# Kernel tuning notes

Measured on AMD Instinct MI355X. Metric: run time of the kernel, lower is better.

Reference implementation:

```python
import jax, jax.numpy as jnp
import numpy as np

N_NODES = 50000
N_EDGES = 800000
IN_FEATS = 256
H_FEATS = 256
NUM_CLASSES = 16
NUM_GRAPHS = 64


def _glorot(key, shape):
    lim = float(np.sqrt(6.0 / (shape[0] + shape[1])))
    return jax.random.uniform(key, shape, jnp.float32, -lim, lim)


def setup_inputs() -> dict:
    key = jax.random.key(0)
    ks = jax.random.split(key, 12)
    x = jax.random.normal(ks[0], (N_NODES, IN_FEATS), jnp.float32)
    edge_index = jax.random.randint(ks[1], (2, N_EDGES), 0, N_NODES, jnp.int64)
    batch_vec = jnp.sort(jax.random.randint(ks[2], (N_NODES,), 0, NUM_GRAPHS, jnp.int64))
    W1 = _glorot(ks[3], (IN_FEATS, H_FEATS)); b1 = jnp.zeros((H_FEATS,), jnp.float32)
    W2 = _glorot(ks[4], (H_FEATS, H_FEATS)); b2 = jnp.zeros((H_FEATS,), jnp.float32)
    W3 = _glorot(ks[5], (H_FEATS, H_FEATS)); b3 = jnp.zeros((H_FEATS,), jnp.float32)
    W4 = _glorot(ks[6], (H_FEATS, NUM_CLASSES)); b4 = jnp.zeros((NUM_CLASSES,), jnp.float32)
    return {"x": x, "edge_index": edge_index, "batch_vec": batch_vec,
            "W1": W1, "b1": b1, "W2": W2, "b2": b2,
            "W3": W3, "b3": b3, "W4": W4, "b4": b4}


def gcn_conv(x, W, b, src, dst, deg_inv_sqrt):
    # PyG GCNConv: out = D^{-1/2} (A + I) D^{-1/2} (x W) + b
    h = x @ W  # [N, F_out]
    norm = deg_inv_sqrt[src] * deg_inv_sqrt[dst]  # [E+N]
    msgs = h[src] * norm[:, None]  # gather + scale
    agg = jax.ops.segment_sum(msgs, dst, num_segments=x.shape[0])
    return agg + b


def reference(x, edge_index, batch_vec, W1, b1, W2, b2, W3, b3, W4, b4):
    n = x.shape[0]
    # add self-loops once (shared across layers)
    loops = jnp.arange(n, dtype=edge_index.dtype)
    src = jnp.concatenate([edge_index[0], loops])
    dst = jnp.concatenate([edge_index[1], loops])
    deg = jax.ops.segment_sum(jnp.ones_like(dst, dtype=x.dtype), dst, num_segments=n)
    deg_inv_sqrt = jnp.where(deg > 0, jax.lax.rsqrt(deg), 0.0)

    h = gcn_conv(x, W1, b1, src, dst, deg_inv_sqrt)
    h_copy = jax.nn.relu(h)
    # dropout is identity in eval mode (training=False)
    h = gcn_conv(h_copy, W2, b2, src, dst, deg_inv_sqrt)
    h_copy = jax.nn.relu(jax.nn.relu(h) + h_copy)
    h = gcn_conv(h_copy, W3, b3, src, dst, deg_inv_sqrt)
    h = jax.nn.relu(jax.nn.relu(h) + h_copy)
    h = gcn_conv(h, W4, b4, src, dst, deg_inv_sqrt)

    # global_mean_pool over batch vector
    sums = jax.ops.segment_sum(h, batch_vec, num_segments=NUM_GRAPHS)
    counts = jax.ops.segment_sum(jnp.ones((n,), h.dtype), batch_vec, num_segments=NUM_GRAPHS)
    return sums / jnp.maximum(counts, 1.0)[:, None]
```

## Files before the change

kernel.cpp:

```cpp
#include <hip/hip_runtime.h>
#include <hip/hip_bf16.h>

#define N_NODES 50000
#define N_EDGES 800000
#define F 256
#define NGRAPH 64
#define NCLS 16
#define NBLK_N 196

typedef short short8 __attribute__((ext_vector_type(8)));
typedef float f32x4 __attribute__((ext_vector_type(4)));

__device__ __forceinline__ float bf2f(ushort u) {
    unsigned v = ((unsigned)u) << 16;
    return __uint_as_float(v);
}
__device__ __forceinline__ ushort f2bf(float f) {
    __hip_bfloat16 b = __float2bfloat16(f);
    return *reinterpret_cast<ushort*>(&b);
}
__device__ __forceinline__ float bflo(uint u) { return __uint_as_float(u << 16); }
__device__ __forceinline__ float bfhi(uint u) { return __uint_as_float(u & 0xffff0000u); }


__global__ __launch_bounds__(256) void k_init(int* __restrict__ ecnt,
                                              float* __restrict__ pool,
                                              float* __restrict__ cnt) {
    int i = blockIdx.x * 256 + threadIdx.x;
    if (i < N_NODES) ecnt[i] = 0;
    if (i < NGRAPH * NCLS) pool[i] = 0.f;
    if (i < NGRAPH) cnt[i] = 0.f;
}

__global__ __launch_bounds__(256) void k_count(const int* __restrict__ dst,
                                               int* __restrict__ ecnt) {
    int e = blockIdx.x * 256 + threadIdx.x;
    if (e < N_EDGES) atomicAdd(&ecnt[dst[e]], 1);
}

__global__ __launch_bounds__(256) void k_scan_block(const int* __restrict__ ecnt,
                                                    int* __restrict__ rowptr,
                                                    int* __restrict__ blkSum,
                                                    float* __restrict__ dinv) {
    __shared__ int sh[256];
    int i = blockIdx.x * 256 + threadIdx.x;
    int v = (i < N_NODES) ? ecnt[i] : 0;
    sh[threadIdx.x] = v;
    __syncthreads();
#pragma unroll
    for (int off = 1; off < 256; off <<= 1) {
        int t = (threadIdx.x >= off) ? sh[threadIdx.x - off] : 0;
        __syncthreads();
        sh[threadIdx.x] += t;
        __syncthreads();
    }
    if (i < N_NODES) {
        rowptr[i] = sh[threadIdx.x] - v;
        dinv[i] = rsqrtf((float)(v + 1));
    }
    if (threadIdx.x == 255) blkSum[blockIdx.x] = sh[255];
}

__global__ __launch_bounds__(256) void k_scan_add(const int* __restrict__ blkSum,
                                                  int* __restrict__ rowptr,
                                                  int* __restrict__ cursor) {
    __shared__ int sh[256];
    int t = threadIdx.x;
    sh[t] = (t < NBLK_N && t < (int)blockIdx.x) ? blkSum[t] : 0;
    __syncthreads();
#pragma unroll
    for (int off = 128; off > 0; off >>= 1) {
        if (t < off) sh[t] += sh[t + off];
        __syncthreads();
    }
    int base = sh[0];
    int i = blockIdx.x * 256 + t;
    if (i < N_NODES) {
        int r = rowptr[i] + base;
        rowptr[i] = r;
        cursor[i] = r;
    }
    if (i == 0) rowptr[N_NODES] = N_EDGES;
}

__global__ __launch_bounds__(256) void k_fill_csr(const int* __restrict__ src,
                                                  const int* __restrict__ dst,
                                                  int* __restrict__ cursor,
                                                  ushort* __restrict__ csr16) {
    int e = blockIdx.x * 256 + threadIdx.x;
    if (e >= N_EDGES) return;
    int s = src[e];
    int d = dst[e];
    int p = atomicAdd(&cursor[d], 1);
    csr16[p] = (ushort)s;
}


__global__ __launch_bounds__(256) void k_wpack3(const float* __restrict__ W1,
                                                const float* __restrict__ W2,
                                                const float* __restrict__ W3,
                                                ushort* __restrict__ Wp) {
    int gid = blockIdx.x * 256 + threadIdx.x;
    int which = gid >> 13;
    int idx = gid & 8191;
    const float* W = (which == 0) ? W1 : (which == 1) ? W2 : W3;
    ushort* o = Wp + (size_t)which * 65536;
    int lane = idx & 63;
    int ks = (idx >> 6) & 7;
    int ctg = idx >> 9;
    int kbase = ks * 32 + (lane >> 4) * 8;
    int col = ctg * 16 + (lane & 15);
    short8 v;
#pragma unroll
    for (int e = 0; e < 8; ++e)
        v[e] = (short)f2bf(W[(size_t)(kbase + e) * 256 + col]);
    *(short8*)(o + (size_t)idx * 8) = v;
}


template <int F32IN>
__global__ __launch_bounds__(256, 2) void k_mfma256(const void* __restrict__ Av,
                                                    const ushort* __restrict__ Wp,
                                                    const float* __restrict__ dinv,
                                                    ushort* __restrict__ C) {
    __shared__ __align__(16) ushort cs[4][16 * 72];
    const int t = threadIdx.x;
    const int wv = t >> 6;
    const int l = t & 63;
    const int m0 = blockIdx.x * 32;
    const int colbase = wv * 64;
    const int lrow = l & 15;
    const int lk = (l >> 4) * 8;

    short8 wf[4][8];
    const short8* wp = (const short8*)Wp;
#pragma unroll
    for (int ct = 0; ct < 4; ++ct)
#pragma unroll
        for (int ks = 0; ks < 8; ++ks)
            wf[ct][ks] = wp[(size_t)(((wv * 4 + ct) * 8 + ks) * 64) + l];

#pragma unroll
    for (int msub = 0; msub < 2; ++msub) {
        int arow = m0 + msub * 16 + lrow;
        if (arow >= N_NODES) arow = N_NODES - 1;
        short8 af[8];
        if (F32IN) {
            const float* ap = (const float*)Av + (size_t)arow * F + lk;
#pragma unroll
            for (int ks = 0; ks < 8; ++ks) {
                float4 a0 = *(const float4*)(ap + ks * 32);
                float4 a1 = *(const float4*)(ap + ks * 32 + 4);
                af[ks][0] = (short)f2bf(a0.x); af[ks][1] = (short)f2bf(a0.y);
                af[ks][2] = (short)f2bf(a0.z); af[ks][3] = (short)f2bf(a0.w);
                af[ks][4] = (short)f2bf(a1.x); af[ks][5] = (short)f2bf(a1.y);
                af[ks][6] = (short)f2bf(a1.z); af[ks][7] = (short)f2bf(a1.w);
            }
        } else {
            const ushort* ap = (const ushort*)Av + (size_t)arow * F + lk;
#pragma unroll
            for (int ks = 0; ks < 8; ++ks)
                af[ks] = *(const short8*)(ap + ks * 32);
        }

        f32x4 acc[4];
#pragma unroll
        for (int ct = 0; ct < 4; ++ct) acc[ct] = (f32x4){0.f, 0.f, 0.f, 0.f};
#pragma unroll
        for (int ks = 0; ks < 8; ++ks)
#pragma unroll
            for (int ct = 0; ct < 4; ++ct)
                acc[ct] = __builtin_amdgcn_mfma_f32_16x16x32_bf16(af[ks], wf[ct][ks], acc[ct], 0, 0, 0);

        int orow0 = m0 + msub * 16 + (l >> 4) * 4;
        float dv[4];
#pragma unroll
        for (int r = 0; r < 4; ++r)
            dv[r] = (orow0 + r < N_NODES) ? dinv[orow0 + r] : 0.f;

#pragma unroll
        for (int ct = 0; ct < 4; ++ct) {
            int col = ct * 16 + (l & 15);
#pragma unroll
            for (int r = 0; r < 4; ++r) {
                int row = (l >> 4) * 4 + r;
                cs[wv][row * 72 + col] = f2bf(acc[ct][r] * dv[r]);
            }
        }
#pragma unroll
        for (int h = 0; h < 2; ++h) {
            int row = h * 8 + (l >> 3);
            int coff = (l & 7) * 8;
            short8 v = *(const short8*)&cs[wv][row * 72 + coff];
            int orow = m0 + msub * 16 + row;
            if (orow < N_NODES)
                *(short8*)(C + (size_t)orow * F + colbase + coff) = v;
        }
    }
}


template <int MODE>
__global__ __launch_bounds__(256) void k_gather256(const ushort* __restrict__ H,
                                                   const float* __restrict__ bias,
                                                   const float* __restrict__ dinv,
                                                   const int* __restrict__ rowptr,
                                                   const ushort* __restrict__ csr16,
                                                   const ushort* __restrict__ hc,
                                                   ushort* __restrict__ OUT) {
    int gid = blockIdx.x * 256 + threadIdx.x;
    int n = gid >> 6;
    int lane = gid & 63;
    if (n >= N_NODES) return;
    const int slot = lane >> 5;
    const int c = (lane & 31) * 8;

    float acc[8];
#pragma unroll
    for (int j = 0; j < 8; ++j) acc[j] = 0.f;

    int i = rowptr[n] + slot;
    const int end = rowptr[n + 1];
    for (; i + 6 < end; i += 8) {
        int s0 = csr16[i], s1 = csr16[i + 2], s2 = csr16[i + 4], s3 = csr16[i + 6];
        short8 v0 = *(const short8*)(H + (size_t)s0 * F + c);
        short8 v1 = *(const short8*)(H + (size_t)s1 * F + c);
        short8 v2 = *(const short8*)(H + (size_t)s2 * F + c);
        short8 v3 = *(const short8*)(H + (size_t)s3 * F + c);
#pragma unroll
        for (int j = 0; j < 8; ++j)
            acc[j] += (bf2f((ushort)v0[j]) + bf2f((ushort)v1[j])) +
                      (bf2f((ushort)v2[j]) + bf2f((ushort)v3[j]));
    }
    for (; i < end; i += 2) {
        int s0 = csr16[i];
        short8 v0 = *(const short8*)(H + (size_t)s0 * F + c);
#pragma unroll
        for (int j = 0; j < 8; ++j) acc[j] += bf2f((ushort)v0[j]);
    }

#pragma unroll
    for (int j = 0; j < 8; ++j) acc[j] += __shfl_xor(acc[j], 32);

    if (slot == 0) {
        const short8 h = *(const short8*)(H + (size_t)n * F + c);
        const float4 b0 = *(const float4*)(bias + c);
        const float4 b1 = *(const float4*)(bias + c + 4);
        float bb[8] = {b0.x, b0.y, b0.z, b0.w, b1.x, b1.y, b1.z, b1.w};
        float di = dinv[n];
        float s[8];
#pragma unroll
        for (int j = 0; j < 8; ++j)
            s[j] = bb[j] + di * (acc[j] + bf2f((ushort)h[j]));

        short8 ov;
        if (MODE == 1) {
#pragma unroll
            for (int j = 0; j < 8; ++j)
                ov[j] = (short)f2bf(fmaxf(s[j], 0.f));
        } else {
            const short8 hv = *(const short8*)(hc + (size_t)n * F + c);
#pragma unroll
            for (int j = 0; j < 8; ++j)
                ov[j] = (short)f2bf(fmaxf(fmaxf(s[j], 0.f) + bf2f((ushort)hv[j]), 0.f));
        }
        *(short8*)(OUT + (size_t)n * F + c) = ov;
    }
}


__global__ __launch_bounds__(256) void k_gemm16(const ushort* __restrict__ A,
                                                const float* __restrict__ W4,
                                                const float* __restrict__ dinv,
                                                ushort* __restrict__ C) {
    __shared__ float Ws[256][16];
    const int t = threadIdx.x;
    {
        const float4* wp = (const float4*)(W4 + (size_t)t * 16);
        float4 a = wp[0], b = wp[1], c = wp[2], d = wp[3];
        float4* sp = (float4*)&Ws[t][0];
        sp[0] = a; sp[1] = b; sp[2] = c; sp[3] = d;
    }
    __syncthreads();
    int row = blockIdx.x * 256 + t;
    if (row >= N_NODES) return;
    const short8* ap = (const short8*)(A + (size_t)row * F);
    float acc[16];
#pragma unroll
    for (int c = 0; c < 16; ++c) acc[c] = 0.f;
    for (int k8 = 0; k8 < 32; ++k8) {
        short8 a8 = ap[k8];
#pragma unroll
        for (int j = 0; j < 8; ++j) {
            float av = bf2f((ushort)a8[j]);
            const float4* wr = (const float4*)&Ws[k8 * 8 + j][0];
            float4 w0 = wr[0], w1 = wr[1], w2 = wr[2], w3 = wr[3];
            acc[0]  += av * w0.x; acc[1]  += av * w0.y;
            acc[2]  += av * w0.z; acc[3]  += av * w0.w;
            acc[4]  += av * w1.x; acc[5]  += av * w1.y;
            acc[6]  += av * w1.z; acc[7]  += av * w1.w;
            acc[8]  += av * w2.x; acc[9]  += av * w2.y;
            acc[10] += av * w2.z; acc[11] += av * w2.w;
            acc[12] += av * w3.x; acc[13] += av * w3.y;
            acc[14] += av * w3.z; acc[15] += av * w3.w;
        }
    }
    float dv = dinv[row];
    short8 o0, o1;
#pragma unroll
    for (int c = 0; c < 8; ++c) o0[c] = (short)f2bf(acc[c] * dv);
#pragma unroll
    for (int c = 0; c < 8; ++c) o1[c] = (short)f2bf(acc[8 + c] * dv);
    short8* op = (short8*)(C + (size_t)row * 16);
    op[0] = o0; op[1] = o1;
}


__global__ __launch_bounds__(256) void k_g16pool(const ushort* __restrict__ G16,
                                                 const float* __restrict__ bias,
                                                 const float* __restrict__ dinv,
                                                 const int* __restrict__ rowptr,
                                                 const ushort* __restrict__ csr16,
                                                 const int* __restrict__ batch,
                                                 float* __restrict__ pool,
                                                 float* __restrict__ cnt) {
    __shared__ float ps[NGRAPH][NCLS];
    __shared__ float pc[NGRAPH];
    for (int i = threadIdx.x; i < NGRAPH * NCLS; i += 256) ((float*)ps)[i] = 0.f;
    if (threadIdx.x < NGRAPH) pc[threadIdx.x] = 0.f;
    __syncthreads();

    int gid = blockIdx.x * 256 + threadIdx.x;
    int n = gid >> 2;
    int q = (gid & 3) * 4;
    if (n < N_NODES) {
        float ax = 0.f, ay = 0.f, az = 0.f, aw = 0.f;
        const int end = rowptr[n + 1];
        for (int i = rowptr[n]; i < end; ++i) {
            int s0 = csr16[i];
            const uint2 u = *(const uint2*)(G16 + (size_t)s0 * 16 + q);
            ax += bflo(u.x); ay += bfhi(u.x);
            az += bflo(u.y); aw += bfhi(u.y);
        }
        const uint2 hu = *(const uint2*)(G16 + (size_t)n * 16 + q);
        const float4 b = *(const float4*)(bias + q);
        float di = dinv[n];
        int g = batch[n];
        atomicAdd(&ps[g][q + 0], b.x + di * (ax + bflo(hu.x)));
        atomicAdd(&ps[g][q + 1], b.y + di * (ay + bfhi(hu.x)));
        atomicAdd(&ps[g][q + 2], b.z + di * (az + bflo(hu.y)));
        atomicAdd(&ps[g][q + 3], b.w + di * (aw + bfhi(hu.y)));
        if ((gid & 3) == 0) atomicAdd(&pc[g], 1.f);
    }
    __syncthreads();

    for (int i = threadIdx.x; i < NGRAPH * NCLS; i += 256) {
        float v = ((float*)ps)[i];
        if (v != 0.f) unsafeAtomicAdd(&pool[i], v);
    }
    if (threadIdx.x < NGRAPH) {
        float v = pc[threadIdx.x];
        if (v > 0.f) unsafeAtomicAdd(&cnt[threadIdx.x], v);
    }
}

__global__ __launch_bounds__(256) void k_final(const float* __restrict__ pool,
                                               const float* __restrict__ cnt,
                                               float* __restrict__ out) {
    int i = blockIdx.x * 256 + threadIdx.x;
    if (i < NGRAPH * NCLS) out[i] = pool[i] / fmaxf(cnt[i >> 4], 1.f);
}


extern "C" void kernel_launch(void* const* d_in, const int* in_sizes, int n_in,
                              void* d_out, int out_size, void* d_ws, size_t ws_size,
                              hipStream_t stream) {
    const float* x   = (const float*)d_in[0];
    const int*   ei  = (const int*)d_in[1];
    const int*   bvec= (const int*)d_in[2];
    const float* W1  = (const float*)d_in[3];
    const float* b1  = (const float*)d_in[4];
    const float* W2  = (const float*)d_in[5];
    const float* b2  = (const float*)d_in[6];
    const float* W3  = (const float*)d_in[7];
    const float* b3  = (const float*)d_in[8];
    const float* W4  = (const float*)d_in[9];
    const float* b4  = (const float*)d_in[10];
    float* out = (float*)d_out;

    const int* src = ei;
    const int* dst = ei + N_EDGES;

    const size_t NF = (size_t)N_NODES * F;
    ushort* P   = (ushort*)d_ws;
    ushort* Q   = P + NF;
    ushort* Hg  = Q + NF;
    ushort* G16 = Hg + NF;
    float*  aux = (float*)(G16 + (size_t)N_NODES * 16 + 64);
    int*    ecnt   = (int*)aux;
    float*  dinv   = aux + N_NODES;
    int*    rowptr = (int*)(aux + 2 * N_NODES);
    int*    cursor = (int*)(aux + 3 * N_NODES + 64);
    int*    blkSum = (int*)(aux + 4 * N_NODES + 64);
    ushort* csr16  = (ushort*)(blkSum + 256);
    float*  pool   = (float*)(csr16 + N_EDGES);
    float*  cnt    = pool + NGRAPH * NCLS;
    ushort* Wp     = (ushort*)(cnt + NGRAPH);

    const int BN = NBLK_N;
    const int BE = (N_EDGES + 255) / 256;
    const int BM = (N_NODES + 31) / 32;
    const int BG = (N_NODES * 64 + 255) / 256;
    const int B4 = (N_NODES * 4 + 255) / 256;

    k_init<<<BN, 256, 0, stream>>>(ecnt, pool, cnt);
    k_count<<<BE, 256, 0, stream>>>(dst, ecnt);
    k_scan_block<<<BN, 256, 0, stream>>>(ecnt, rowptr, blkSum, dinv);
    k_scan_add<<<BN, 256, 0, stream>>>(blkSum, rowptr, cursor);
    k_fill_csr<<<BE, 256, 0, stream>>>(src, dst, cursor, csr16);

    k_wpack3<<<96, 256, 0, stream>>>(W1, W2, W3, Wp);

    k_mfma256<1><<<BM, 256, 0, stream>>>(x, Wp, dinv, Hg);
    k_gather256<1><<<BG, 256, 0, stream>>>(Hg, b1, dinv, rowptr, csr16, nullptr, P);

    k_mfma256<0><<<BM, 256, 0, stream>>>(P, Wp + 65536, dinv, Hg);
    k_gather256<2><<<BG, 256, 0, stream>>>(Hg, b2, dinv, rowptr, csr16, P, Q);

    k_mfma256<0><<<BM, 256, 0, stream>>>(Q, Wp + 131072, dinv, Hg);
    k_gather256<2><<<BG, 256, 0, stream>>>(Hg, b3, dinv, rowptr, csr16, Q, P);

    k_gemm16<<<BN, 256, 0, stream>>>(P, W4, dinv, G16);
    k_g16pool<<<B4, 256, 0, stream>>>(G16, b4, dinv, rowptr, csr16, bvec, pool, cnt);

    k_final<<<4, 256, 0, stream>>>(pool, cnt, out);
}
```

Baseline: 399.2 us.

## Fuse neighbor aggregation into GEMM by aggregating before multiplying with weights

Reorders each GCN layer to aggregate neighbor features first, (A·X)·W, and fuses the gather with the MFMA GEMM in a single kernel per layer. Aggregated rows go into shared memory as the GEMM A operand. Activations are stored pre-scaled by D^{-1/2}, and sqrt(deg) is used to undo this for the residual, which drops the separate gather kernels and the intermediate Hg round trip. In exchange, weight fragments are now reloaded per column tile instead of kept in registers, occupancy may fall from the added shared memory and the gather loop, and the extra bf16 rounding of scaled values changes numerics slightly.

```diff
diff --git a/kernel.cpp b/kernel.cpp
--- a/kernel.cpp
+++ b/kernel.cpp
@@ -41,7 +41,8 @@
 __global__ __launch_bounds__(256) void k_scan_block(const int* __restrict__ ecnt,
                                                     int* __restrict__ rowptr,
                                                     int* __restrict__ blkSum,
-                                                    float* __restrict__ dinv) {
+                                                    float* __restrict__ dinv,
+                                                    float* __restrict__ sdeg) {
     __shared__ int sh[256];
     int i = blockIdx.x * 256 + threadIdx.x;
     int v = (i < N_NODES) ? ecnt[i] : 0;
@@ -56,7 +57,9 @@
     }
     if (i < N_NODES) {
         rowptr[i] = sh[threadIdx.x] - v;
-        dinv[i] = rsqrtf((float)(v + 1));
+        float d = (float)(v + 1);
+        dinv[i] = rsqrtf(d);
+        sdeg[i] = sqrtf(d);
     }
     if (threadIdx.x == 255) blkSum[blockIdx.x] = sh[255];
 }
@@ -93,6 +96,24 @@
     int d = dst[e];
     int p = atomicAdd(&cursor[d], 1);
     csr16[p] = (ushort)s;
+}
+
+
+__global__ __launch_bounds__(256) void k_prescale(const float* __restrict__ x,
+                                                  const float* __restrict__ dinv,
+                                                  ushort* __restrict__ T0) {
+    int i = blockIdx.x * 256 + threadIdx.x;
+    if (i >= (int)((size_t)N_NODES * F / 8)) return;
+    int n = i >> 5;
+    float di = dinv[n];
+    const float4* ip = (const float4*)(x + (size_t)i * 8);
+    float4 a = ip[0], b = ip[1];
+    short8 v;
+    v[0] = (short)f2bf(a.x * di); v[1] = (short)f2bf(a.y * di);
+    v[2] = (short)f2bf(a.z * di); v[3] = (short)f2bf(a.w * di);
+    v[4] = (short)f2bf(b.x * di); v[5] = (short)f2bf(b.y * di);
+    v[6] = (short)f2bf(b.z * di); v[7] = (short)f2bf(b.w * di);
+    *(short8*)(T0 + (size_t)i * 8) = v;
 }
 
 
@@ -118,160 +139,145 @@
 }
 
 
-template <int F32IN>
-__global__ __launch_bounds__(256, 2) void k_mfma256(const void* __restrict__ Av,
-                                                    const ushort* __restrict__ Wp,
-                                                    const float* __restrict__ dinv,
-                                                    ushort* __restrict__ C) {
+template <int MODE>
+__global__ __launch_bounds__(256) void k_layer(const ushort* __restrict__ Hs,
+                                               const ushort* __restrict__ Wp,
+                                               const float* __restrict__ bias,
+                                               const float* __restrict__ dinv,
+                                               const float* __restrict__ sdeg,
+                                               const int* __restrict__ rowptr,
+                                               const ushort* __restrict__ csr16,
+                                               ushort* __restrict__ OUT) {
+    __shared__ __align__(16) ushort At[32 * 264];
     __shared__ __align__(16) ushort cs[4][16 * 72];
     const int t = threadIdx.x;
     const int wv = t >> 6;
     const int l = t & 63;
     const int m0 = blockIdx.x * 32;
+
+    {
+        const int slot = l >> 5;
+        const int c = (l & 31) * 8;
+        for (int rep = 0; rep < 8; ++rep) {
+            const int noderow = wv * 8 + rep;
+            const int n = m0 + noderow;
+            const bool valid = n < N_NODES;
+            const int nn = valid ? n : 0;
+
+            float acc[8];
+#pragma unroll
+            for (int j = 0; j < 8; ++j) acc[j] = 0.f;
+
+            int i = valid ? rowptr[nn] + slot : 0;
+            const int end = valid ? rowptr[nn + 1] : 0;
+            for (; i + 6 < end; i += 8) {
+                int s0 = csr16[i], s1 = csr16[i + 2], s2 = csr16[i + 4], s3 = csr16[i + 6];
+                short8 v0 = *(const short8*)(Hs + (size_t)s0 * F + c);
+                short8 v1 = *(const short8*)(Hs + (size_t)s1 * F + c);
+                short8 v2 = *(const short8*)(Hs + (size_t)s2 * F + c);
+                short8 v3 = *(const short8*)(Hs + (size_t)s3 * F + c);
+#pragma unroll
+                for (int j = 0; j < 8; ++j)
+                    acc[j] += (bf2f((ushort)v0[j]) + bf2f((ushort)v1[j])) +
+                              (bf2f((ushort)v2[j]) + bf2f((ushort)v3[j]));
+            }
+            for (; i < end; i += 2) {
+                int s0 = csr16[i];
+                short8 v0 = *(const short8*)(Hs + (size_t)s0 * F + c);
+#pragma unroll
+                for (int j = 0; j < 8; ++j) acc[j] += bf2f((ushort)v0[j]);
+            }
+
+#pragma unroll
+            for (int j = 0; j < 8; ++j) acc[j] += __shfl_xor(acc[j], 32);
+
+            if (slot == 0) {
+                short8 av;
+                if (valid) {
+                    const short8 h = *(const short8*)(Hs + (size_t)nn * F + c);
+                    float di = dinv[nn];
+#pragma unroll
+                    for (int j = 0; j < 8; ++j)
+                        av[j] = (short)f2bf(di * (acc[j] + bf2f((ushort)h[j])));
+                } else {
+#pragma unroll
+                    for (int j = 0; j < 8; ++j) av[j] = 0;
+                }
+                *(short8*)&At[noderow * 264 + c] = av;
+            }
+        }
+    }
+    __syncthreads();
+
     const int colbase = wv * 64;
     const int lrow = l & 15;
     const int lk = (l >> 4) * 8;
-
-    short8 wf[4][8];
     const short8* wp = (const short8*)Wp;
-#pragma unroll
-    for (int ct = 0; ct < 4; ++ct)
+
+#pragma unroll
+    for (int msub = 0; msub < 2; ++msub) {
+        short8 af[8];
 #pragma unroll
         for (int ks = 0; ks < 8; ++ks)
-            wf[ct][ks] = wp[(size_t)(((wv * 4 + ct) * 8 + ks) * 64) + l];
-
-#pragma unroll
-    for (int msub = 0; msub < 2; ++msub) {
-        int arow = m0 + msub * 16 + lrow;
-        if (arow >= N_NODES) arow = N_NODES - 1;
-        short8 af[8];
-        if (F32IN) {
-            const float* ap = (const float*)Av + (size_t)arow * F + lk;
-#pragma unroll
-            for (int ks = 0; ks < 8; ++ks) {
-                float4 a0 = *(const float4*)(ap + ks * 32);
-                float4 a1 = *(const float4*)(ap + ks * 32 + 4);
-                af[ks][0] = (short)f2bf(a0.x); af[ks][1] = (short)f2bf(a0.y);
-                af[ks][2] = (short)f2bf(a0.z); af[ks][3] = (short)f2bf(a0.w);
-                af[ks][4] = (short)f2bf(a1.x); af[ks][5] = (short)f2bf(a1.y);
-                af[ks][6] = (short)f2bf(a1.z); af[ks][7] = (short)f2bf(a1.w);
-            }
-        } else {
-            const ushort* ap = (const ushort*)Av + (size_t)arow * F + lk;
+            af[ks] = *(const short8*)&At[(msub * 16 + lrow) * 264 + lk + ks * 32];
+
+#pragma unroll
+        for (int ct = 0; ct < 4; ++ct) {
+            short8 wf[8];
 #pragma unroll
             for (int ks = 0; ks < 8; ++ks)
-                af[ks] = *(const short8*)(ap + ks * 32);
-        }
-
-        f32x4 acc[4];
-#pragma unroll
-        for (int ct = 0; ct < 4; ++ct) acc[ct] = (f32x4){0.f, 0.f, 0.f, 0.f};
-#pragma unroll
-        for (int ks = 0; ks < 8; ++ks)
-#pragma unroll
-            for (int ct = 0; ct < 4; ++ct)
-                acc[ct] = __builtin_amdgcn_mfma_f32_16x16x32_bf16(af[ks], wf[ct][ks], acc[ct], 0, 0, 0);
-
-        int orow0 = m0 + msub * 16 + (l >> 4) * 4;
-        float dv[4];
-#pragma unroll
-        for (int r = 0; r < 4; ++r)
-            dv[r] = (orow0 + r < N_NODES) ? dinv[orow0 + r] : 0.f;
-
-#pragma unroll
-        for (int ct = 0; ct < 4; ++ct) {
+                wf[ks] = wp[(size_t)(((wv * 4 + ct) * 8 + ks) * 64) + l];
+
+            f32x4 acc = (f32x4){0.f, 0.f, 0.f, 0.f};
+#pragma unroll
+            for (int ks = 0; ks < 8; ++ks)
+                acc = __builtin_amdgcn_mfma_f32_16x16x32_bf16(af[ks], wf[ks], acc, 0, 0, 0);
+
             int col = ct * 16 + (l & 15);
 #pragma unroll
             for (int r = 0; r < 4; ++r) {
                 int row = (l >> 4) * 4 + r;
-                cs[wv][row * 72 + col] = f2bf(acc[ct][r] * dv[r]);
+                cs[wv][row * 72 + col] = f2bf(acc[r]);
             }
         }
 #pragma unroll
         for (int h = 0; h < 2; ++h) {
             int row = h * 8 + (l >> 3);
             int coff = (l & 7) * 8;
-            short8 v = *(const short8*)&cs[wv][row * 72 + coff];
             int orow = m0 + msub * 16 + row;
-            if (orow < N_NODES)
-                *(short8*)(C + (size_t)orow * F + colbase + coff) = v;
+            if (orow < N_NODES) {
+                short8 z8 = *(const short8*)&cs[wv][row * 72 + coff];
+                int gcol = colbase + coff;
+                const float4 b0 = *(const float4*)(bias + gcol);
+                const float4 b1 = *(const float4*)(bias + gcol + 4);
+                float bb[8] = {b0.x, b0.y, b0.z, b0.w, b1.x, b1.y, b1.z, b1.w};
+                float di = dinv[orow];
+                short8 ov;
+                if (MODE == 2) {
+                    const short8 hp = *(const short8*)(Hs + (size_t)orow * F + gcol);
+                    float sd = sdeg[orow];
+#pragma unroll
+                    for (int j = 0; j < 8; ++j) {
+                        float u = fmaxf(bf2f((ushort)z8[j]) + bb[j], 0.f);
+                        u = fmaxf(u + bf2f((ushort)hp[j]) * sd, 0.f);
+                        ov[j] = (short)f2bf(u * di);
+                    }
+                } else {
+#pragma unroll
+                    for (int j = 0; j < 8; ++j) {
+                        float u = fmaxf(bf2f((ushort)z8[j]) + bb[j], 0.f);
+                        ov[j] = (short)f2bf(u * di);
+                    }
+                }
+                *(short8*)(OUT + (size_t)orow * F + gcol) = ov;
+            }
         }
-    }
-}
-
-
-template <int MODE>
-__global__ __launch_bounds__(256) void k_gather256(const ushort* __restrict__ H,
-                                                   const float* __restrict__ bias,
-                                                   const float* __restrict__ dinv,
-                                                   const int* __restrict__ rowptr,
-                                                   const ushort* __restrict__ csr16,
-                                                   const ushort* __restrict__ hc,
-                                                   ushort* __restrict__ OUT) {
-    int gid = blockIdx.x * 256 + threadIdx.x;
-    int n = gid >> 6;
-    int lane = gid & 63;
-    if (n >= N_NODES) return;
-    const int slot = lane >> 5;
-    const int c = (lane & 31) * 8;
-
-    float acc[8];
-#pragma unroll
-    for (int j = 0; j < 8; ++j) acc[j] = 0.f;
-
-    int i = rowptr[n] + slot;
-    const int end = rowptr[n + 1];
-    for (; i + 6 < end; i += 8) {
-        int s0 = csr16[i], s1 = csr16[i + 2], s2 = csr16[i + 4], s3 = csr16[i + 6];
-        short8 v0 = *(const short8*)(H + (size_t)s0 * F + c);
-        short8 v1 = *(const short8*)(H + (size_t)s1 * F + c);
-        short8 v2 = *(const short8*)(H + (size_t)s2 * F + c);
-        short8 v3 = *(const short8*)(H + (size_t)s3 * F + c);
-#pragma unroll
-        for (int j = 0; j < 8; ++j)
-            acc[j] += (bf2f((ushort)v0[j]) + bf2f((ushort)v1[j])) +
-                      (bf2f((ushort)v2[j]) + bf2f((ushort)v3[j]));
-    }
-    for (; i < end; i += 2) {
-        int s0 = csr16[i];
-        short8 v0 = *(const short8*)(H + (size_t)s0 * F + c);
-#pragma unroll
-        for (int j = 0; j < 8; ++j) acc[j] += bf2f((ushort)v0[j]);
-    }
-
-#pragma unroll
-    for (int j = 0; j < 8; ++j) acc[j] += __shfl_xor(acc[j], 32);
-
-    if (slot == 0) {
-        const short8 h = *(const short8*)(H + (size_t)n * F + c);
-        const float4 b0 = *(const float4*)(bias + c);
-        const float4 b1 = *(const float4*)(bias + c + 4);
-        float bb[8] = {b0.x, b0.y, b0.z, b0.w, b1.x, b1.y, b1.z, b1.w};
-        float di = dinv[n];
-        float s[8];
-#pragma unroll
-        for (int j = 0; j < 8; ++j)
-            s[j] = bb[j] + di * (acc[j] + bf2f((ushort)h[j]));
-
-        short8 ov;
-        if (MODE == 1) {
-#pragma unroll
-            for (int j = 0; j < 8; ++j)
-                ov[j] = (short)f2bf(fmaxf(s[j], 0.f));
-        } else {
-            const short8 hv = *(const short8*)(hc + (size_t)n * F + c);
-#pragma unroll
-            for (int j = 0; j < 8; ++j)
-                ov[j] = (short)f2bf(fmaxf(fmaxf(s[j], 0.f) + bf2f((ushort)hv[j]), 0.f));
-        }
-        *(short8*)(OUT + (size_t)n * F + c) = ov;
     }
 }
 
 
 __global__ __launch_bounds__(256) void k_gemm16(const ushort* __restrict__ A,
                                                 const float* __restrict__ W4,
-                                                const float* __restrict__ dinv,
                                                 ushort* __restrict__ C) {
     __shared__ float Ws[256][16];
     const int t = threadIdx.x;
@@ -305,12 +311,11 @@
             acc[14] += av * w3.z; acc[15] += av * w3.w;
         }
     }
-    float dv = dinv[row];
     short8 o0, o1;
 #pragma unroll
-    for (int c = 0; c < 8; ++c) o0[c] = (short)f2bf(acc[c] * dv);
-#pragma unroll
-    for (int c = 0; c < 8; ++c) o1[c] = (short)f2bf(acc[8 + c] * dv);
+    for (int c = 0; c < 8; ++c) o0[c] = (short)f2bf(acc[c]);
+#pragma unroll
+    for (int c = 0; c < 8; ++c) o1[c] = (short)f2bf(acc[8 + c]);
     short8* op = (short8*)(C + (size_t)row * 16);
     op[0] = o0; op[1] = o1;
 }
@@ -392,16 +397,17 @@
     const int* dst = ei + N_EDGES;
 
     const size_t NF = (size_t)N_NODES * F;
-    ushort* P   = (ushort*)d_ws;
-    ushort* Q   = P + NF;
-    ushort* Hg  = Q + NF;
-    ushort* G16 = Hg + NF;
+    ushort* T0  = (ushort*)d_ws;
+    ushort* T1  = T0 + NF;
+    ushort* T2  = T1 + NF;
+    ushort* G16 = T2 + NF;
     float*  aux = (float*)(G16 + (size_t)N_NODES * 16 + 64);
     int*    ecnt   = (int*)aux;
     float*  dinv   = aux + N_NODES;
-    int*    rowptr = (int*)(aux + 2 * N_NODES);
-    int*    cursor = (int*)(aux + 3 * N_NODES + 64);
-    int*    blkSum = (int*)(aux + 4 * N_NODES + 64);
+    float*  sdeg   = aux + 2 * N_NODES;
+    int*    rowptr = (int*)(aux + 3 * N_NODES);
+    int*    cursor = (int*)(aux + 4 * N_NODES + 64);
+    int*    blkSum = (int*)(aux + 5 * N_NODES + 64);
     ushort* csr16  = (ushort*)(blkSum + 256);
     float*  pool   = (float*)(csr16 + N_EDGES);
     float*  cnt    = pool + NGRAPH * NCLS;
@@ -409,28 +415,24 @@
 
     const int BN = NBLK_N;
     const int BE = (N_EDGES + 255) / 256;
-    const int BM = (N_NODES + 31) / 32;
-    const int BG = (N_NODES * 64 + 255) / 256;
+    const int BL = (N_NODES + 31) / 32;
     const int B4 = (N_NODES * 4 + 255) / 256;
+    const int BP = (int)((NF / 8 + 255) / 256);
 
     k_init<<<BN, 256, 0, stream>>>(ecnt, pool, cnt);
     k_count<<<BE, 256, 0, stream>>>(dst, ecnt);
-    k_scan_block<<<BN, 256, 0, stream>>>(ecnt, rowptr, blkSum, dinv);
+    k_scan_block<<<BN, 256, 0, stream>>>(ecnt, rowptr, blkSum, dinv, sdeg);
     k_scan_add<<<BN, 256, 0, stream>>>(blkSum, rowptr, cursor);
     k_fill_csr<<<BE, 256, 0, stream>>>(src, dst, cursor, csr16);
 
     k_wpack3<<<96, 256, 0, stream>>>(W1, W2, W3, Wp);
-
-    k_mfma256<1><<<BM, 256, 0, stream>>>(x, Wp, dinv, Hg);
-    k_gather256<1><<<BG, 256, 0, stream>>>(Hg, b1, dinv, rowptr, csr16, nullptr, P);
-
-    k_mfma256<0><<<BM, 256, 0, stream>>>(P, Wp + 65536, dinv, Hg);
-    k_gather256<2><<<BG, 256, 0, stream>>>(Hg, b2, dinv, rowptr, csr16, P, Q);
-
-    k_mfma256<0><<<BM, 256, 0, stream>>>(Q, Wp + 131072, dinv, Hg);
-    k_gather256<2><<<BG, 256, 0, stream>>>(Hg, b3, dinv, rowptr, csr16, Q, P);
-
-    k_gemm16<<<BN, 256, 0, stream>>>(P, W4, dinv, G16);
+    k_prescale<<<BP, 256, 0, stream>>>(x, dinv, T0);
+
+    k_layer<1><<<BL, 256, 0, stream>>>(T0, Wp,          b1, dinv, sdeg, rowptr, csr16, T1);
+    k_layer<2><<<BL, 256, 0, stream>>>(T1, Wp + 65536,  b2, dinv, sdeg, rowptr, csr16, T2);
+    k_layer<2><<<BL, 256, 0, stream>>>(T2, Wp + 131072, b3, dinv, sdeg, rowptr, csr16, T0);
+
+    k_gemm16<<<BN, 256, 0, stream>>>(T0, W4, G16);
     k_g16pool<<<B4, 256, 0, stream>>>(G16, b4, dinv, rowptr, csr16, bvec, pool, cnt);
 
     k_final<<<4, 256, 0, stream>>>(pool, cnt, out);
```

Result: slower. 427.2 us (+7.0%).
